# Kernel optimization log

Measured on AMD Instinct MI355X. Metric: run time of the kernel, lower is better.

## Reference

```python
import jax, jax.numpy as jnp
import numpy as np

K = 20
EPS = 1e-5

def knn_idx(x, k):
    # x: (B, N, C). Returns indices of k nearest neighbors (by squared L2), (B, N, k).
    inner = jnp.einsum('bnc,bmc->bnm', x, x)
    sq = jnp.sum(x * x, axis=-1)  # (B, N)
    neg_dist = 2.0 * inner - sq[:, :, None] - sq[:, None, :]
    return jax.lax.top_k(neg_dist, k)[1]

def bn(x, gamma, beta, axes):
    # BatchNorm in training mode (batch statistics, biased variance), eps=1e-5.
    m = jnp.mean(x, axis=axes, keepdims=True)
    v = jnp.var(x, axis=axes, keepdims=True)
    return (x - m) * jax.lax.rsqrt(v + EPS) * gamma + beta

def lrelu(x):
    return jnp.where(x >= 0, x, 0.2 * x)

def edge_conv(x, W, g, b):
    # x: (B, N, C); W: (O, 2C). EdgeConv: knn gather -> concat(nbr-ctr, ctr) -> 1x1 conv -> BN -> LReLU -> max over k.
    B = x.shape[0]
    idx = knn_idx(x, K)                                   # (B, N, K)
    nbr = x[jnp.arange(B)[:, None, None], idx]            # (B, N, K, C)
    ctr = jnp.broadcast_to(x[:, :, None, :], nbr.shape)
    e = jnp.concatenate([nbr - ctr, ctr], axis=-1)        # (B, N, K, 2C)
    h = jnp.einsum('bnkc,oc->bnko', e, W)
    h = lrelu(bn(h, g, b, (0, 1, 2)))
    return jnp.max(h, axis=2)                             # (B, N, O)

def _forward(data, W1, g1, b1, W2, g2, b2, W3, g3, b3, W4, g4, b4,
             W5, g5, b5, fc1W, bn1g, bn1b, fc2W, fc2b, bn2g, bn2b, fc3W, fc3b):
    x = jnp.transpose(data, (0, 2, 1))                    # (B, N, 3)
    d1 = edge_conv(x,  W1, g1, b1)                        # (B, N, 64)
    d2 = edge_conv(d1, W2, g2, b2)                        # (B, N, 64)
    d3 = edge_conv(d2, W3, g3, b3)                        # (B, N, 128)
    d4 = edge_conv(d3, W4, g4, b4)                        # (B, N, 256)
    cat = jnp.concatenate([d1, d2, d3, d4], axis=-1)      # (B, N, 512)
    h = lrelu(bn(jnp.einsum('bnc,oc->bno', cat, W5), g5, b5, (0, 1)))  # (B, N, 1024)
    f = jnp.concatenate([jnp.max(h, axis=1), jnp.mean(h, axis=1)], axis=-1)  # (B, 2048)
    f = lrelu(bn(f @ fc1W.T, bn1g, bn1b, (0,)))           # dropout = identity (eval)
    f = lrelu(bn(f @ fc2W.T + fc2b, bn2g, bn2b, (0,)))
    return f @ fc3W.T + fc3b                              # (B, numClass)

def setup_inputs() -> dict:
    key = jax.random.key(0)
    ks = jax.random.split(key, 16)
    B, N, emb, ncls = 16, 2048, 1024, 40
    s = 0.05
    inp = {
        'data': jax.random.normal(ks[0], (B, 3, N), dtype=jnp.float32),
        'W1': jax.random.normal(ks[1], (64, 6), dtype=jnp.float32) * s,
        'g1': jnp.ones((64,), jnp.float32), 'b1': jnp.zeros((64,), jnp.float32),
        'W2': jax.random.normal(ks[2], (64, 128), dtype=jnp.float32) * s,
        'g2': jnp.ones((64,), jnp.float32), 'b2': jnp.zeros((64,), jnp.float32),
        'W3': jax.random.normal(ks[3], (128, 128), dtype=jnp.float32) * s,
        'g3': jnp.ones((128,), jnp.float32), 'b3': jnp.zeros((128,), jnp.float32),
        'W4': jax.random.normal(ks[4], (256, 256), dtype=jnp.float32) * s,
        'g4': jnp.ones((256,), jnp.float32), 'b4': jnp.zeros((256,), jnp.float32),
        'W5': jax.random.normal(ks[5], (emb, 512), dtype=jnp.float32) * s,
        'g5': jnp.ones((emb,), jnp.float32), 'b5': jnp.zeros((emb,), jnp.float32),
        'fc1W': jax.random.normal(ks[6], (512, emb * 2), dtype=jnp.float32) * s,
        'bn1g': jnp.ones((512,), jnp.float32), 'bn1b': jnp.zeros((512,), jnp.float32),
        'fc2W': jax.random.normal(ks[7], (256, 512), dtype=jnp.float32) * s,
        'fc2b': jnp.zeros((256,), jnp.float32),
        'bn2g': jnp.ones((256,), jnp.float32), 'bn2b': jnp.zeros((256,), jnp.float32),
        'fc3W': jax.random.normal(ks[8], (ncls, 256), dtype=jnp.float32) * s,
        'fc3b': jnp.zeros((ncls,), jnp.float32),
    }
    return inp

def reference(data, W1, g1, b1, W2, g2, b2, W3, g3, b3, W4, g4, b4,
              W5, g5, b5, fc1W, bn1g, bn1b, fc2W, fc2b, bn2g, bn2b, fc3W, fc3b):
    return _forward(data, W1, g1, b1, W2, g2, b2, W3, g3, b3, W4, g4, b4,
                    W5, g5, b5, fc1W, bn1g, bn1b, fc2W, fc2b, bn2g, bn2b, fc3W, fc3b)
```

## Files before the change

### kernel.cpp

```cpp
#include <hip/hip_runtime.h>
#include <math.h>

#define LRELU(x) ((x) >= 0.f ? (x) : 0.2f*(x))

typedef _Float16 f16;
typedef f16 f16x8 __attribute__((ext_vector_type(8)));
typedef f16 f16x4 __attribute__((ext_vector_type(4)));
typedef float f32x4 __attribute__((ext_vector_type(4)));

#define WS_FLOATS 78000000u
__device__ __align__(256) float g_ws[WS_FLOATS];

__global__ __launch_bounds__(256) void k_transpose_in(const float* __restrict__ data,
                                                      float* __restrict__ x0) {
    int i = blockIdx.x*256 + threadIdx.x;
    int b = i >> 11, n = i & 2047;
    #pragma unroll
    for (int c = 0; c < 3; c++)
        x0[(long)i*3 + c] = data[((long)b*3 + c)*2048 + n];
}

__global__ __launch_bounds__(256) void k_sqnorm(const float* __restrict__ x,
                                                float* __restrict__ sq, int C) {
    int i = blockIdx.x*256 + threadIdx.x;
    const float* xr = x + (long)i*C;
    float s = 0.f;
    for (int c = 0; c < C; c++) s = fmaf(xr[c], xr[c], s);
    sq[i] = s;
}

#define KC 8
__global__ __launch_bounds__(256) void k_gemm_nt(
    const float* __restrict__ A, int lda, long sAb,
    const float* __restrict__ B, int ldb, long sBb,
    float* __restrict__ Cm, int ldc, long sCb,
    int K, int Nj, int mode, const float* __restrict__ sq, int sqStride)
{
    __shared__ float As[KC][132];
    __shared__ float Bs[KC][132];
    int z = blockIdx.z;
    const float* Ab = A + (long)z*sAb;
    const float* Bb = B + (long)z*sBb;
    float* Cb = Cm + (long)z*sCb;
    int rowBase = blockIdx.x*128, colBase = blockIdx.y*128;
    int tid = threadIdx.x, tx = tid & 15, ty = tid >> 4;
    float acc[8][8] = {};
    for (int k0 = 0; k0 < K; k0 += KC) {
        #pragma unroll
        for (int l = 0; l < 4; l++) {
            int id = tid + l*256;
            int kk = id & 7, r = id >> 3;
            float av = 0.f, bv = 0.f;
            if (k0 + kk < K) {
                av = Ab[(long)(rowBase + r)*lda + k0 + kk];
                if (colBase + r < Nj)
                    bv = Bb[(long)(colBase + r)*ldb + k0 + kk];
            }
            As[kk][r] = av; Bs[kk][r] = bv;
        }
        __syncthreads();
        #pragma unroll
        for (int kk = 0; kk < KC; kk++) {
            float4 a0 = *(const float4*)&As[kk][ty*8];
            float4 a1 = *(const float4*)&As[kk][ty*8 + 4];
            float4 b0 = *(const float4*)&Bs[kk][tx*4];
            float4 b1 = *(const float4*)&Bs[kk][64 + tx*4];
            float a[8] = {a0.x,a0.y,a0.z,a0.w,a1.x,a1.y,a1.z,a1.w};
            float b[8] = {b0.x,b0.y,b0.z,b0.w,b1.x,b1.y,b1.z,b1.w};
            #pragma unroll
            for (int i = 0; i < 8; i++)
                #pragma unroll
                for (int j = 0; j < 8; j++)
                    acc[i][j] = fmaf(a[i], b[j], acc[i][j]);
        }
        __syncthreads();
    }
    const float* sqz = sq + (long)z*sqStride;
    #pragma unroll
    for (int i = 0; i < 8; i++) {
        int r = rowBase + ty*8 + i;
        float sqr = (mode == 2) ? sqz[r] : 0.f;
        #pragma unroll
        for (int half = 0; half < 2; half++) {
            int c = colBase + half*64 + tx*4;
            int jb = half*4;
            if (c + 3 < Nj) {
                float4 v;
                v.x = acc[i][jb+0]; v.y = acc[i][jb+1];
                v.z = acc[i][jb+2]; v.w = acc[i][jb+3];
                if (mode == 2) {
                    v.x = 2.f*v.x - sqr - sqz[c+0];
                    v.y = 2.f*v.y - sqr - sqz[c+1];
                    v.z = 2.f*v.z - sqr - sqz[c+2];
                    v.w = 2.f*v.w - sqr - sqz[c+3];
                }
                *(float4*)&Cb[(long)r*ldc + c] = v;
            } else {
                #pragma unroll
                for (int j = 0; j < 4; j++) {
                    int c2 = c + j;
                    if (c2 >= Nj) continue;
                    float v = acc[i][jb+j];
                    if (mode == 2) v = 2.f*v - sqr - sqz[c2];
                    Cb[(long)r*ldc + c2] = v;
                }
            }
        }
    }
}

__global__ __launch_bounds__(256) void k_gemm_mfma_nt(
    const f16* __restrict__ A, int lda,
    const f16* __restrict__ Bm, int ldb,
    float* __restrict__ Cm, int ldc, int K)
{
    __shared__ f16 As[128][40];
    __shared__ f16 Bs[128][40];
    int t = threadIdx.x;
    int rowBase = blockIdx.x*128, colBase = blockIdx.y*128;
    int wave = t >> 6, l = t & 63;
    int wrow = (wave >> 1)*64, wcol = (wave & 1)*64;
    int lr = l & 15, kg = l >> 4;
    int sr = t >> 1, seg = (t & 1)*16;

    f32x4 acc[4][4] = {};
    for (int k0 = 0; k0 < K; k0 += 32) {
        const f16* ga = A  + (long)(rowBase + sr)*lda + k0 + seg;
        const f16* gb = Bm + (long)(colBase + sr)*ldb + k0 + seg;
        uint4 a0 = *(const uint4*)ga;
        uint4 a1 = *(const uint4*)(ga + 8);
        uint4 b0 = *(const uint4*)gb;
        uint4 b1 = *(const uint4*)(gb + 8);
        *(uint4*)&As[sr][seg]     = a0;
        *(uint4*)&As[sr][seg + 8] = a1;
        *(uint4*)&Bs[sr][seg]     = b0;
        *(uint4*)&Bs[sr][seg + 8] = b1;
        __syncthreads();
        f16x8 af[4], bf[4];
        #pragma unroll
        for (int i = 0; i < 4; i++) af[i] = *(const f16x8*)&As[wrow + i*16 + lr][kg*8];
        #pragma unroll
        for (int j = 0; j < 4; j++) bf[j] = *(const f16x8*)&Bs[wcol + j*16 + lr][kg*8];
        #pragma unroll
        for (int i = 0; i < 4; i++)
            #pragma unroll
            for (int j = 0; j < 4; j++)
                acc[i][j] = __builtin_amdgcn_mfma_f32_16x16x32_f16(af[i], bf[j], acc[i][j], 0, 0, 0);
        __syncthreads();
    }
    #pragma unroll
    for (int i = 0; i < 4; i++) {
        #pragma unroll
        for (int j = 0; j < 4; j++) {
            int row = rowBase + wrow + i*16 + kg*4;
            int col = colBase + wcol + j*16 + lr;
            #pragma unroll
            for (int r2 = 0; r2 < 4; r2++)
                Cm[(long)(row + r2)*ldc + col] = acc[i][j][r2];
        }
    }
}

__global__ __launch_bounds__(256) void k_cvt_f16(const float* __restrict__ in,
                                                 f16* __restrict__ out, int n) {
    int i = blockIdx.x*256 + threadIdx.x;
    if (i < n) out[i] = (f16)in[i];
}

__global__ __launch_bounds__(256) void k_topk20(const float* __restrict__ dist,
                                                int* __restrict__ idxOut, int rowOffset)
{
    __shared__ float lds[4][2048];
    int wave = threadIdx.x >> 6, lane = threadIdx.x & 63;
    int row = blockIdx.x*4 + wave;
    const float* dr = dist + (long)row*2048;
    float* L = lds[wave];
    for (int i = 0; i < 32; i++) L[i*64 + lane] = dr[i*64 + lane];
    __syncthreads();
    int* out = idxOut + (long)(rowOffset + row)*20;
    for (int it = 0; it < 20; it++) {
        float bv = -INFINITY; int bi = 0x7fffffff;
        for (int i = 0; i < 32; i++) {
            float v = L[i*64 + lane];
            if (v > bv) { bv = v; bi = i*64 + lane; }
        }
        #pragma unroll
        for (int s = 32; s > 0; s >>= 1) {
            float ov = __shfl_xor(bv, s);
            int   oi = __shfl_xor(bi, s);
            if (ov > bv || (ov == bv && oi < bi)) { bv = ov; bi = oi; }
        }
        if (lane == 0) out[it] = bi;
        if (lane == (bi & 63)) L[bi] = -INFINITY;
    }
}

__global__ __launch_bounds__(256) void k_wdiff(const float* __restrict__ W,
                                               float* __restrict__ Wd, int O, int C) {
    int i = blockIdx.x*256 + threadIdx.x;
    if (i >= O*C) return;
    int o = i / C, c = i % C;
    Wd[o*C + c] = W[(long)o*2*C + C + c] - W[(long)o*2*C + c];
}

__global__ __launch_bounds__(256) void k_edge_gather(
    const float* __restrict__ p, const float* __restrict__ q,
    const int* __restrict__ idx,
    float* __restrict__ hmax, float* __restrict__ hmin,
    float* __restrict__ partial, int O, int lg2TPP)
{
    __shared__ float ldsS[1024];
    __shared__ float ldsS2[1024];
    int tid = threadIdx.x;
    int TPP = O >> 2;
    int c4 = (tid & (TPP - 1)) << 2;
    int sub = tid >> lg2TPP;
    int nsub = 256 >> lg2TPP;
    int wg = blockIdx.x;
    int logical = (wg & 7)*256 + (wg >> 3);
    int base = logical*16;
    float4 s = {0,0,0,0}, s2 = {0,0,0,0};
    int iters = 16 / nsub;
    for (int it = 0; it < iters; ++it) {
        int pt = base + sub + it*nsub;
        int bb = (pt >> 11) << 11;
        const int* ir = idx + (long)pt*20;
        float4 qv = *(const float4*)&q[(long)pt*O + c4];
        float4 mx = {-INFINITY,-INFINITY,-INFINITY,-INFINITY};
        float4 mn = { INFINITY, INFINITY, INFINITY, INFINITY};
        for (int k = 0; k < 20; ++k) {
            int m = ir[k];
            float4 pv = *(const float4*)&p[(long)(bb + m)*O + c4];
            float4 h;
            h.x = pv.x + qv.x; h.y = pv.y + qv.y;
            h.z = pv.z + qv.z; h.w = pv.w + qv.w;
            mx.x = fmaxf(mx.x, h.x); mx.y = fmaxf(mx.y, h.y);
            mx.z = fmaxf(mx.z, h.z); mx.w = fmaxf(mx.w, h.w);
            mn.x = fminf(mn.x, h.x); mn.y = fminf(mn.y, h.y);
            mn.z = fminf(mn.z, h.z); mn.w = fminf(mn.w, h.w);
            s.x += h.x; s.y += h.y; s.z += h.z; s.w += h.w;
            s2.x = fmaf(h.x, h.x, s2.x); s2.y = fmaf(h.y, h.y, s2.y);
            s2.z = fmaf(h.z, h.z, s2.z); s2.w = fmaf(h.w, h.w, s2.w);
        }
        *(float4*)&hmax[(long)pt*O + c4] = mx;
        *(float4*)&hmin[(long)pt*O + c4] = mn;
    }
    *(float4*)&ldsS [sub*O + c4] = s;
    *(float4*)&ldsS2[sub*O + c4] = s2;
    __syncthreads();
    if (tid < O) {
        float a = 0.f, b = 0.f;
        for (int u = 0; u < nsub; ++u) { a += ldsS[u*O + tid]; b += ldsS2[u*O + tid]; }
        partial[(long)wg*2*O + tid] = a;
        partial[(long)wg*2*O + O + tid] = b;
    }
}

__global__ __launch_bounds__(256) void k_colsum(const float* __restrict__ partial,
                                                float* __restrict__ out, int W, int rpc) {
    int c = blockIdx.x*256 + threadIdx.x;
    if (c >= W) return;
    long r0 = (long)blockIdx.y * rpc;
    float s = 0.f;
    for (int r = 0; r < rpc; ++r) s += partial[(r0 + r)*W + c];
    out[(long)blockIdx.y*W + c] = s;
}

__global__ __launch_bounds__(256) void k_bn_finalize(
    const float* __restrict__ sums, const float* __restrict__ g,
    const float* __restrict__ beta, float* __restrict__ ss, int O, float invCnt)
{
    int o = blockIdx.x*256 + threadIdx.x;
    if (o >= O) return;
    float mean = sums[o]*invCnt;
    float var  = sums[O + o]*invCnt - mean*mean;
    float sc = g[o] * rsqrtf(var + 1e-5f);
    ss[o] = sc;
    ss[O + o] = beta[o] - mean*sc;
}

__global__ __launch_bounds__(256) void k_edge_apply(
    const float* __restrict__ hmax, const float* __restrict__ hmin,
    const float* __restrict__ ss, float* __restrict__ out, int O,
    f16* __restrict__ catH, int co, int lg2O)
{
    long i4 = (long)blockIdx.x*256 + threadIdx.x;
    int c4 = (int)(i4 & ((O >> 2) - 1)) << 2;
    int pt = (int)(i4 >> (lg2O - 2));
    float4 mx = *(const float4*)&hmax[i4*4];
    float4 mn = *(const float4*)&hmin[i4*4];
    float4 y;
    {
        float sc = ss[c4+0], sh = ss[O+c4+0];
        float v = fmaf(sc >= 0.f ? mx.x : mn.x, sc, sh); y.x = LRELU(v);
    }
    {
        float sc = ss[c4+1], sh = ss[O+c4+1];
        float v = fmaf(sc >= 0.f ? mx.y : mn.y, sc, sh); y.y = LRELU(v);
    }
    {
        float sc = ss[c4+2], sh = ss[O+c4+2];
        float v = fmaf(sc >= 0.f ? mx.z : mn.z, sc, sh); y.z = LRELU(v);
    }
    {
        float sc = ss[c4+3], sh = ss[O+c4+3];
        float v = fmaf(sc >= 0.f ? mx.w : mn.w, sc, sh); y.w = LRELU(v);
    }
    *(float4*)&out[i4*4] = y;
    f16x4 hv;
    hv[0] = (f16)y.x; hv[1] = (f16)y.y; hv[2] = (f16)y.z; hv[3] = (f16)y.w;
    *(f16x4*)&catH[(long)pt*512 + co + c4] = hv;
}

__global__ __launch_bounds__(256) void k_h5_stats_p(const float* __restrict__ h5,
                                                    float* __restrict__ partial) {
    int tid = threadIdx.x, bid = blockIdx.x;
    int base = bid*16;
    float s[4] = {0,0,0,0}, s2[4] = {0,0,0,0};
    for (int i = 0; i < 16; ++i) {
        long row = (long)(base + i)*1024;
        #pragma unroll
        for (int cc = 0; cc < 4; ++cc) {
            float v = h5[row + cc*256 + tid];
            s[cc] += v; s2[cc] = fmaf(v, v, s2[cc]);
        }
    }
    #pragma unroll
    for (int cc = 0; cc < 4; ++cc) {
        partial[(long)bid*2048 + cc*256 + tid] = s[cc];
        partial[(long)bid*2048 + 1024 + cc*256 + tid] = s2[cc];
    }
}

__global__ __launch_bounds__(256) void k_reduce_fp(const float* __restrict__ h5,
                                                   const float* __restrict__ ss,
                                                   float* __restrict__ fpart) {
    int b = blockIdx.x, ch = blockIdx.y;
    int c = blockIdx.z*256 + threadIdx.x;
    float sc = ss[c], sh = ss[1024 + c];
    float mx = -INFINITY, sm = 0.f;
    int n0 = ch*128;
    for (int n = n0; n < n0 + 128; ++n) {
        float v = h5[((long)(b*2048 + n))*1024 + c];
        float y = fmaf(v, sc, sh); y = LRELU(y);
        mx = fmaxf(mx, y); sm += y;
    }
    fpart[((long)(b*16 + ch))*2048 + c] = mx;
    fpart[((long)(b*16 + ch))*2048 + 1024 + c] = sm;
}

__global__ __launch_bounds__(256) void k_reduce_ff(const float* __restrict__ fpart,
                                                   float* __restrict__ f) {
    int b = blockIdx.x;
    int c = blockIdx.y*256 + threadIdx.x;
    float mx = -INFINITY, sm = 0.f;
    for (int ch = 0; ch < 16; ++ch) {
        mx = fmaxf(mx, fpart[((long)(b*16 + ch))*2048 + c]);
        sm += fpart[((long)(b*16 + ch))*2048 + 1024 + c];
    }
    f[(long)b*2048 + c] = mx;
    f[(long)b*2048 + 1024 + c] = sm * (1.f/2048.f);
}

__global__ __launch_bounds__(256) void k_fc_wave(const float* __restrict__ X,
                                                 const float* __restrict__ W,
                                                 const float* __restrict__ bias,
                                                 float* __restrict__ Y,
                                                 int Kdim, int Ncol) {
    int wid = blockIdx.x*4 + (threadIdx.x >> 6);
    int lane = threadIdx.x & 63;
    if (wid >= 16*Ncol) return;
    int b = wid / Ncol, j = wid % Ncol;
    const float* xr = X + (long)b*Kdim;
    const float* wr = W + (long)j*Kdim;
    float s = 0.f;
    for (int k = lane*4; k < Kdim; k += 256) {
        float4 xv = *(const float4*)&xr[k];
        float4 wv = *(const float4*)&wr[k];
        s = fmaf(xv.x, wv.x, s); s = fmaf(xv.y, wv.y, s);
        s = fmaf(xv.z, wv.z, s); s = fmaf(xv.w, wv.w, s);
    }
    #pragma unroll
    for (int sft = 32; sft > 0; sft >>= 1) s += __shfl_xor(s, sft);
    if (lane == 0) Y[wid] = s + (bias ? bias[j] : 0.f);
}

__global__ __launch_bounds__(256) void k_bn_rows(const float* __restrict__ X,
                                                 const float* __restrict__ g,
                                                 const float* __restrict__ be,
                                                 float* __restrict__ Y, int Ncol) {
    int j = blockIdx.x*256 + threadIdx.x;
    if (j >= Ncol) return;
    float s = 0.f, s2 = 0.f;
    for (int b = 0; b < 16; b++) { float v = X[b*Ncol + j]; s += v; s2 = fmaf(v, v, s2); }
    float mean = s*(1.f/16.f);
    float var  = s2*(1.f/16.f) - mean*mean;
    float sc = g[j]*rsqrtf(var + 1e-5f);
    float sh = be[j] - mean*sc;
    for (int b = 0; b < 16; b++) {
        float v = fmaf(X[b*Ncol + j], sc, sh);
        Y[b*Ncol + j] = LRELU(v);
    }
}

extern "C" void kernel_launch(void* const* d_in, const int* in_sizes, int n_in,
                              void* d_out, int out_size, void* d_ws, size_t ws_size,
                              hipStream_t stream) {
    const float* data = (const float*)d_in[0];
    const float* W1 = (const float*)d_in[1];  const float* g1 = (const float*)d_in[2];  const float* b1 = (const float*)d_in[3];
    const float* W2 = (const float*)d_in[4];  const float* g2 = (const float*)d_in[5];  const float* b2 = (const float*)d_in[6];
    const float* W3 = (const float*)d_in[7];  const float* g3 = (const float*)d_in[8];  const float* b3 = (const float*)d_in[9];
    const float* W4 = (const float*)d_in[10]; const float* g4 = (const float*)d_in[11]; const float* b4 = (const float*)d_in[12];
    const float* W5 = (const float*)d_in[13]; const float* g5 = (const float*)d_in[14]; const float* b5 = (const float*)d_in[15];
    const float* fc1W = (const float*)d_in[16]; const float* bn1g = (const float*)d_in[17]; const float* bn1b = (const float*)d_in[18];
    const float* fc2W = (const float*)d_in[19]; const float* fc2b = (const float*)d_in[20];
    const float* bn2g = (const float*)d_in[21]; const float* bn2b = (const float*)d_in[22];
    const float* fc3W = (const float*)d_in[23]; const float* fc3b = (const float*)d_in[24];

    void* wsym = nullptr;
    hipGetSymbolAddress(&wsym, HIP_SYMBOL(g_ws));
    char* w = (char*)wsym;
    size_t off = 0;
    auto alloc = [&](size_t bytes) { void* r = w + off; off += (bytes + 255) & ~size_t(255); return r; };
    float* S   = (float*)alloc(134217728);
    float* x0  = (float*)alloc(393216);
    float* d1  = (float*)alloc(8388608);
    float* d2  = (float*)alloc(8388608);
    float* d3  = (float*)alloc(16777216);
    float* d4  = (float*)alloc(33554432);
    float* p   = (float*)alloc(33554432);
    float* q   = (float*)alloc(33554432);
    int*   idxb= (int*)  alloc(2621440);
    float* sqb = (float*)alloc(131072);
    float* Wd  = (float*)alloc(131072);
    float* sums= (float*)alloc(8192);
    float* ssb = (float*)alloc(8192);
    float* f   = (float*)alloc(131072);
    float* t1  = (float*)alloc(32768);
    float* a1  = (float*)alloc(32768);
    float* t2  = (float*)alloc(16384);
    float* a2  = (float*)alloc(16384);
    f16*  catH = (f16*) alloc(33554432);
    f16*  W5H  = (f16*) alloc(1048576);
    (void)ws_size; (void)n_in; (void)in_sizes; (void)out_size; (void)d_ws;

    float* hmaxb = S;
    float* hminb = S + 8388608;
    float* partb = S + 16777216;
    float* part2 = S + 18874368;
    float* h5par = d4;
    float* h5pt2 = d2;
    float* fpart = d1;

    k_transpose_in<<<128, 256, 0, stream>>>(data, x0);

    auto layer = [&](const float* x, int C, int O, int lg2TPP, int lg2O, int co,
                     const float* W, const float* g, const float* beta, float* out) {
        k_sqnorm<<<128, 256, 0, stream>>>(x, sqb, C);
        for (int ch = 0; ch < 4; ch++) {
            const float* xc = x + (long)ch*8192*C;
            k_gemm_nt<<<dim3(16,16,4), 256, 0, stream>>>(
                xc, C, (long)2048*C, xc, C, (long)2048*C,
                S, 2048, (long)2048*2048, C, 2048, 2, sqb + ch*8192, 2048);
            k_topk20<<<2048, 256, 0, stream>>>(S, idxb, ch*8192);
        }
        k_wdiff<<<(O*C + 255)/256, 256, 0, stream>>>(W, Wd, O, C);
        k_gemm_nt<<<dim3(256, (O+127)/128, 1), 256, 0, stream>>>(
            x, C, 0, W, 2*C, 0, p, O, 0, C, O, 0, nullptr, 0);
        k_gemm_nt<<<dim3(256, (O+127)/128, 1), 256, 0, stream>>>(
            x, C, 0, Wd, C, 0, q, O, 0, C, O, 0, nullptr, 0);
        k_edge_gather<<<2048, 256, 0, stream>>>(p, q, idxb, hmaxb, hminb, partb, O, lg2TPP);
        k_colsum<<<dim3((2*O + 255)/256, 32), 256, 0, stream>>>(partb, part2, 2*O, 64);
        k_colsum<<<dim3((2*O + 255)/256, 1),  256, 0, stream>>>(part2, sums,  2*O, 32);
        k_bn_finalize<<<(O+255)/256, 256, 0, stream>>>(sums, g, beta, ssb, O, 1.f/655360.f);
        k_edge_apply<<<32*O, 256, 0, stream>>>(hmaxb, hminb, ssb, out, O, catH, co, lg2O);
    };

    layer(x0, 3,   64,  4, 6, 0,   W1, g1, b1, d1);
    layer(d1, 64,  64,  4, 6, 64,  W2, g2, b2, d2);
    layer(d2, 64,  128, 5, 7, 128, W3, g3, b3, d3);
    layer(d3, 128, 256, 6, 8, 256, W4, g4, b4, d4);

    k_cvt_f16<<<2048, 256, 0, stream>>>(W5, W5H, 524288);
    k_gemm_mfma_nt<<<dim3(256, 8), 256, 0, stream>>>(catH, 512, W5H, 512, S, 1024, 512);

    k_h5_stats_p<<<2048, 256, 0, stream>>>(S, h5par);
    k_colsum<<<dim3(8, 32), 256, 0, stream>>>(h5par, h5pt2, 2048, 64);
    k_colsum<<<dim3(8, 1),  256, 0, stream>>>(h5pt2, sums,  2048, 32);
    k_bn_finalize<<<4, 256, 0, stream>>>(sums, g5, b5, ssb, 1024, 1.f/32768.f);
    k_reduce_fp<<<dim3(16,16,4), 256, 0, stream>>>(S, ssb, fpart);
    k_reduce_ff<<<dim3(16,4), 256, 0, stream>>>(fpart, f);

    k_fc_wave<<<2048, 256, 0, stream>>>(f,  fc1W, nullptr, t1, 2048, 512);
    k_bn_rows<<<2, 256, 0, stream>>>(t1, bn1g, bn1b, a1, 512);
    k_fc_wave<<<1024, 256, 0, stream>>>(a1, fc2W, fc2b, t2, 512, 256);
    k_bn_rows<<<1, 256, 0, stream>>>(t2, bn2g, bn2b, a2, 256);
    k_fc_wave<<<160, 256, 0, stream>>>(a2, fc3W, fc3b, (float*)d_out, 256, 40);
}
```

Baseline: 2.194 ms.

## Fuse kNN distance GEMM with top-k selection in shared memory

Replaces the per-chunk distance GEMM plus separate top-20 kernel with one fused kernel. It computes an 8-row tile of pairwise distances against a transposed copy of x, keeps the tile in LDS and runs the top-k selection there. This removes writing and re-reading the full 2048x2048 distance matrix in global memory, and cuts four chunk launches down to one. The fused GEMM is a plain FMA loop with lower reuse than the tiled GEMM, and it uses 64KB of LDS per block, which limits occupancy. It also adds a transpose kernel and a larger workspace.

Result: slower. 3.864 ms (+76.1%).

```diff
diff --git a/kernel.cpp b/kernel.cpp
--- a/kernel.cpp
+++ b/kernel.cpp
@@ -8,7 +8,7 @@
 typedef f16 f16x4 __attribute__((ext_vector_type(4)));
 typedef float f32x4 __attribute__((ext_vector_type(4)));
 
-#define WS_FLOATS 78000000u
+#define WS_FLOATS 92000000u
 __device__ __align__(256) float g_ws[WS_FLOATS];
 
 __global__ __launch_bounds__(256) void k_transpose_in(const float* __restrict__ data,
@@ -27,6 +27,118 @@
     float s = 0.f;
     for (int c = 0; c < C; c++) s = fmaf(xr[c], xr[c], s);
     sq[i] = s;
+}
+
+__global__ __launch_bounds__(256) void k_transpose_xT(const float* __restrict__ x,
+                                                      float* __restrict__ xT,
+                                                      int C, int KP) {
+    long id = (long)blockIdx.x*256 + threadIdx.x;
+    int n = (int)(id & 2047);
+    long t = id >> 11;
+    int k = (int)(t % KP);
+    int b = (int)(t / KP);
+    xT[((long)b*128 + k)*2048 + n] = (k < C) ? x[((long)(b << 11) + n)*C + k] : 0.f;
+}
+
+__global__ __launch_bounds__(256) void k_knn_fused(
+    const float* __restrict__ x,
+    const float* __restrict__ xT,
+    const float* __restrict__ sq,
+    int* __restrict__ idxOut,
+    int C, int KP)
+{
+    __shared__ float distL[8][2048];
+    int tid = threadIdx.x;
+    int b = blockIdx.y;
+    const float* xTb = xT + (long)b*128*2048;
+    const float* sqb2 = sq + (b << 11);
+    int tx = tid & 15;
+    int ry = tid >> 4;
+    int rp = ry & 3;
+    int g  = ry >> 2;
+    int wave = tid >> 6, lane = tid & 63;
+
+    for (int rb = 0; rb < 8; ++rb) {
+        int rbase = blockIdx.x*64 + rb*8;
+        int r0 = rbase + 2*rp, r1 = r0 + 1;
+        const float* xr0 = x + ((long)(b << 11) + r0)*C;
+        const float* xr1 = x + ((long)(b << 11) + r1)*C;
+        float sqr0 = sqb2[r0], sqr1 = sqb2[r1];
+        for (int ct = 0; ct < 8; ++ct) {
+            int c0 = ct*256 + g*64 + tx*4;
+            float4 acc0 = {0,0,0,0}, acc1 = {0,0,0,0};
+            for (int k0 = 0; k0 < KP; k0 += 8) {
+                float4 bv[8];
+                #pragma unroll
+                for (int kk = 0; kk < 8; ++kk)
+                    bv[kk] = *(const float4*)&xTb[(long)(k0 + kk)*2048 + c0];
+                float a0v[8], a1v[8];
+                if (C >= 8) {
+                    float4 t0 = *(const float4*)&xr0[k0];
+                    float4 t1 = *(const float4*)&xr0[k0 + 4];
+                    a0v[0]=t0.x; a0v[1]=t0.y; a0v[2]=t0.z; a0v[3]=t0.w;
+                    a0v[4]=t1.x; a0v[5]=t1.y; a0v[6]=t1.z; a0v[7]=t1.w;
+                    float4 u0 = *(const float4*)&xr1[k0];
+                    float4 u1 = *(const float4*)&xr1[k0 + 4];
+                    a1v[0]=u0.x; a1v[1]=u0.y; a1v[2]=u0.z; a1v[3]=u0.w;
+                    a1v[4]=u1.x; a1v[5]=u1.y; a1v[6]=u1.z; a1v[7]=u1.w;
+                } else {
+                    #pragma unroll
+                    for (int kk = 0; kk < 8; ++kk) {
+                        int k = k0 + kk;
+                        a0v[kk] = (k < C) ? xr0[k] : 0.f;
+                        a1v[kk] = (k < C) ? xr1[k] : 0.f;
+                    }
+                }
+                #pragma unroll
+                for (int kk = 0; kk < 8; ++kk) {
+                    float4 bb = bv[kk];
+                    acc0.x = fmaf(a0v[kk], bb.x, acc0.x);
+                    acc0.y = fmaf(a0v[kk], bb.y, acc0.y);
+                    acc0.z = fmaf(a0v[kk], bb.z, acc0.z);
+                    acc0.w = fmaf(a0v[kk], bb.w, acc0.w);
+                    acc1.x = fmaf(a1v[kk], bb.x, acc1.x);
+                    acc1.y = fmaf(a1v[kk], bb.y, acc1.y);
+                    acc1.z = fmaf(a1v[kk], bb.z, acc1.z);
+                    acc1.w = fmaf(a1v[kk], bb.w, acc1.w);
+                }
+            }
+            float4 sqc = *(const float4*)&sqb2[c0];
+            float4 d0, d1v;
+            d0.x  = 2.f*acc0.x - sqr0 - sqc.x;
+            d0.y  = 2.f*acc0.y - sqr0 - sqc.y;
+            d0.z  = 2.f*acc0.z - sqr0 - sqc.z;
+            d0.w  = 2.f*acc0.w - sqr0 - sqc.w;
+            d1v.x = 2.f*acc1.x - sqr1 - sqc.x;
+            d1v.y = 2.f*acc1.y - sqr1 - sqc.y;
+            d1v.z = 2.f*acc1.z - sqr1 - sqc.z;
+            d1v.w = 2.f*acc1.w - sqr1 - sqc.w;
+            *(float4*)&distL[2*rp][c0]     = d0;
+            *(float4*)&distL[2*rp + 1][c0] = d1v;
+        }
+        __syncthreads();
+        for (int t = 0; t < 2; ++t) {
+            int r = wave*2 + t;
+            float* L = distL[r];
+            int* out = idxOut + ((long)(b << 11) + rbase + r)*20;
+            for (int it = 0; it < 20; ++it) {
+                float bvv = -INFINITY; int bi = 0x7fffffff;
+                for (int i = 0; i < 32; ++i) {
+                    float v = L[i*64 + lane];
+                    if (v > bvv) { bvv = v; bi = i*64 + lane; }
+                }
+                #pragma unroll
+                for (int s = 32; s > 0; s >>= 1) {
+                    float ov = __shfl_xor(bvv, s);
+                    int   oi = __shfl_xor(bi, s);
+                    if (ov > bvv || (ov == bvv && oi < bi)) { bvv = ov; bi = oi; }
+                }
+                if (lane == 0) out[it] = bi;
+                if (lane == (bi & 63)) L[bi] = -INFINITY;
+            }
+        }
+        __syncthreads();
+    }
 }
 
 #define KC 8
@@ -165,34 +277,6 @@
                                                  f16* __restrict__ out, int n) {
     int i = blockIdx.x*256 + threadIdx.x;
     if (i < n) out[i] = (f16)in[i];
-}
-
-__global__ __launch_bounds__(256) void k_topk20(const float* __restrict__ dist,
-                                                int* __restrict__ idxOut, int rowOffset)
-{
-    __shared__ float lds[4][2048];
-    int wave = threadIdx.x >> 6, lane = threadIdx.x & 63;
-    int row = blockIdx.x*4 + wave;
-    const float* dr = dist + (long)row*2048;
-    float* L = lds[wave];
-    for (int i = 0; i < 32; i++) L[i*64 + lane] = dr[i*64 + lane];
-    __syncthreads();
-    int* out = idxOut + (long)(rowOffset + row)*20;
-    for (int it = 0; it < 20; it++) {
-        float bv = -INFINITY; int bi = 0x7fffffff;
-        for (int i = 0; i < 32; i++) {
-            float v = L[i*64 + lane];
-            if (v > bv) { bv = v; bi = i*64 + lane; }
-        }
-        #pragma unroll
-        for (int s = 32; s > 0; s >>= 1) {
-            float ov = __shfl_xor(bv, s);
-            int   oi = __shfl_xor(bi, s);
-            if (ov > bv || (ov == bv && oi < bi)) { bv = ov; bi = oi; }
-        }
-        if (lane == 0) out[it] = bi;
-        if (lane == (bi & 63)) L[bi] = -INFINITY;
-    }
 }
 
 __global__ __launch_bounds__(256) void k_wdiff(const float* __restrict__ W,
@@ -442,12 +526,14 @@
     float* a2  = (float*)alloc(16384);
     f16*  catH = (f16*) alloc(33554432);
     f16*  W5H  = (f16*) alloc(1048576);
+    float* xT  = (float*)alloc(16777216);
     (void)ws_size; (void)n_in; (void)in_sizes; (void)out_size; (void)d_ws;
 
     float* hmaxb = S;
     float* hminb = S + 8388608;
     float* partb = S + 16777216;
     float* part2 = S + 18874368;
+    float* h5    = S;
     float* h5par = d4;
     float* h5pt2 = d2;
     float* fpart = d1;
@@ -456,14 +542,10 @@
 
     auto layer = [&](const float* x, int C, int O, int lg2TPP, int lg2O, int co,
                      const float* W, const float* g, const float* beta, float* out) {
+        int KP = ((C + 7) >> 3) << 3;
         k_sqnorm<<<128, 256, 0, stream>>>(x, sqb, C);
-        for (int ch = 0; ch < 4; ch++) {
-            const float* xc = x + (long)ch*8192*C;
-            k_gemm_nt<<<dim3(16,16,4), 256, 0, stream>>>(
-                xc, C, (long)2048*C, xc, C, (long)2048*C,
-                S, 2048, (long)2048*2048, C, 2048, 2, sqb + ch*8192, 2048);
-            k_topk20<<<2048, 256, 0, stream>>>(S, idxb, ch*8192);
-        }
+        k_transpose_xT<<<KP*128, 256, 0, stream>>>(x, xT, C, KP);
+        k_knn_fused<<<dim3(32, 16), 256, 0, stream>>>(x, xT, sqb, idxb, C, KP);
         k_wdiff<<<(O*C + 255)/256, 256, 0, stream>>>(W, Wd, O, C);
         k_gemm_nt<<<dim3(256, (O+127)/128, 1), 256, 0, stream>>>(
             x, C, 0, W, 2*C, 0, p, O, 0, C, O, 0, nullptr, 0);
@@ -482,13 +564,13 @@
     layer(d3, 128, 256, 6, 8, 256, W4, g4, b4, d4);
 
     k_cvt_f16<<<2048, 256, 0, stream>>>(W5, W5H, 524288);
-    k_gemm_mfma_nt<<<dim3(256, 8), 256, 0, stream>>>(catH, 512, W5H, 512, S, 1024, 512);
-
-    k_h5_stats_p<<<2048, 256, 0, stream>>>(S, h5par);
+    k_gemm_mfma_nt<<<dim3(256, 8), 256, 0, stream>>>(catH, 512, W5H, 512, h5, 1024, 512);
+
+    k_h5_stats_p<<<2048, 256, 0, stream>>>(h5, h5par);
     k_colsum<<<dim3(8, 32), 256, 0, stream>>>(h5par, h5pt2, 2048, 64);
     k_colsum<<<dim3(8, 1),  256, 0, stream>>>(h5pt2, sums,  2048, 32);
     k_bn_finalize<<<4, 256, 0, stream>>>(sums, g5, b5, ssb, 1024, 1.f/32768.f);
-    k_reduce_fp<<<dim3(16,16,4), 256, 0, stream>>>(S, ssb, fpart);
+    k_reduce_fp<<<dim3(16,16,4), 256, 0, stream>>>(h5, ssb, fpart);
     k_reduce_ff<<<dim3(16,4), 256, 0, stream>>>(fpart, f);
 
     k_fc_wave<<<2048, 256, 0, stream>>>(f,  fc1W, nullptr, t1, 2048, 512);
```

## Fuse distance GEMM with per-tile top-k and add candidate merge kernel

Applied to the files above, without the earlier changes.

Replaces the chunked distance GEMM plus per-row top-k over a full 2048x2048 distance matrix with one fused kernel. Each 128x128 tile computes distances and selects a 20-candidate list per row for its column block using cross-lane shuffles. A second kernel merges the 16 candidate lists (320 entries) per row into the final 20 neighbors. This avoids writing and reading the full distance matrix and the LDS-based scan over 2048 entries, at the cost of 20 serial shuffle-reduction rounds per row inside the GEMM epilogue.

New measurement: 6.251 ms. +184.9%, slower.

```diff
diff --git a/kernel.cpp b/kernel.cpp
--- a/kernel.cpp
+++ b/kernel.cpp
@@ -30,6 +30,119 @@
 }
 
 #define KC 8
+__global__ __launch_bounds__(256) void k_gemm_topk(
+    const float* __restrict__ X, int C, const float* __restrict__ sq,
+    float* __restrict__ candV, int* __restrict__ candI)
+{
+    __shared__ float As[KC][132];
+    __shared__ float Bs[KC][132];
+    int z = blockIdx.z;
+    const float* Ab = X + ((long)z << 11)*C;
+    int rowBase = blockIdx.x*128, colBase = blockIdx.y*128;
+    int tid = threadIdx.x, tx = tid & 15, ty = tid >> 4;
+    float acc[8][8] = {};
+    for (int k0 = 0; k0 < C; k0 += KC) {
+        #pragma unroll
+        for (int l = 0; l < 4; l++) {
+            int id = tid + l*256;
+            int kk = id & 7, r = id >> 3;
+            float av = 0.f, bv = 0.f;
+            if (k0 + kk < C) {
+                av = Ab[(long)(rowBase + r)*C + k0 + kk];
+                bv = Ab[(long)(colBase + r)*C + k0 + kk];
+            }
+            As[kk][r] = av; Bs[kk][r] = bv;
+        }
+        __syncthreads();
+        #pragma unroll
+        for (int kk = 0; kk < KC; kk++) {
+            float4 a0 = *(const float4*)&As[kk][ty*8];
+            float4 a1 = *(const float4*)&As[kk][ty*8 + 4];
+            float4 b0 = *(const float4*)&Bs[kk][tx*4];
+            float4 b1 = *(const float4*)&Bs[kk][64 + tx*4];
+            float a[8] = {a0.x,a0.y,a0.z,a0.w,a1.x,a1.y,a1.z,a1.w};
+            float b[8] = {b0.x,b0.y,b0.z,b0.w,b1.x,b1.y,b1.z,b1.w};
+            #pragma unroll
+            for (int i = 0; i < 8; i++)
+                #pragma unroll
+                for (int j = 0; j < 8; j++)
+                    acc[i][j] = fmaf(a[i], b[j], acc[i][j]);
+        }
+        __syncthreads();
+    }
+    const float* sqz = sq + ((long)z << 11);
+    #pragma unroll
+    for (int i = 0; i < 8; i++) {
+        int rloc = ty*8 + i;
+        float sqr = sqz[rowBase + rloc];
+        float dv[8]; int gi[8];
+        #pragma unroll
+        for (int j = 0; j < 8; j++) {
+            int c = colBase + ((j < 4) ? tx*4 + j : 64 + tx*4 + (j - 4));
+            dv[j] = 2.f*acc[i][j] - sqr - sqz[c];
+            gi[j] = c;
+        }
+        unsigned mask = 0;
+        long obase = (((long)((z << 11) + rowBase + rloc))*16 + blockIdx.y)*20;
+        for (int it = 0; it < 20; it++) {
+            float bv = -INFINITY; int bi = 0x7fffffff;
+            #pragma unroll
+            for (int j = 0; j < 8; j++) {
+                if (!((mask >> j) & 1u)) {
+                    if (dv[j] > bv || (dv[j] == bv && gi[j] < bi)) { bv = dv[j]; bi = gi[j]; }
+                }
+            }
+            #pragma unroll
+            for (int sft = 1; sft < 16; sft <<= 1) {
+                float ov = __shfl_xor(bv, sft);
+                int   oi = __shfl_xor(bi, sft);
+                if (ov > bv || (ov == bv && oi < bi)) { bv = ov; bi = oi; }
+            }
+            #pragma unroll
+            for (int j = 0; j < 8; j++)
+                if (gi[j] == bi) mask |= 1u << j;
+            if (tx == 0) { candV[obase + it] = bv; candI[obase + it] = bi; }
+        }
+    }
+}
+
+__global__ __launch_bounds__(256) void k_topk_merge(
+    const float* __restrict__ candV, const int* __restrict__ candI,
+    int* __restrict__ idxOut)
+{
+    int wave = threadIdx.x >> 6, lane = threadIdx.x & 63;
+    int row = blockIdx.x*4 + wave;
+    const float* cv = candV + (long)row*320;
+    const int*   ci = candI + (long)row*320;
+    float v[5]; int id[5];
+    #pragma unroll
+    for (int u = 0; u < 5; u++) {
+        v[u]  = cv[lane + u*64];
+        id[u] = ci[lane + u*64];
+    }
+    unsigned mask = 0;
+    int* out = idxOut + (long)row*20;
+    for (int it = 0; it < 20; it++) {
+        float bv = -INFINITY; int bi = 0x7fffffff;
+        #pragma unroll
+        for (int u = 0; u < 5; u++) {
+            if (!((mask >> u) & 1u)) {
+                if (v[u] > bv || (v[u] == bv && id[u] < bi)) { bv = v[u]; bi = id[u]; }
+            }
+        }
+        #pragma unroll
+        for (int sft = 32; sft > 0; sft >>= 1) {
+            float ov = __shfl_xor(bv, sft);
+            int   oi = __shfl_xor(bi, sft);
+            if (ov > bv || (ov == bv && oi < bi)) { bv = ov; bi = oi; }
+        }
+        #pragma unroll
+        for (int u = 0; u < 5; u++)
+            if (id[u] == bi) mask |= 1u << u;
+        if (lane == 0) out[it] = bi;
+    }
+}
+
 __global__ __launch_bounds__(256) void k_gemm_nt(
     const float* __restrict__ A, int lda, long sAb,
     const float* __restrict__ B, int ldb, long sBb,
@@ -165,34 +278,6 @@
                                                  f16* __restrict__ out, int n) {
     int i = blockIdx.x*256 + threadIdx.x;
     if (i < n) out[i] = (f16)in[i];
-}
-
-__global__ __launch_bounds__(256) void k_topk20(const float* __restrict__ dist,
-                                                int* __restrict__ idxOut, int rowOffset)
-{
-    __shared__ float lds[4][2048];
-    int wave = threadIdx.x >> 6, lane = threadIdx.x & 63;
-    int row = blockIdx.x*4 + wave;
-    const float* dr = dist + (long)row*2048;
-    float* L = lds[wave];
-    for (int i = 0; i < 32; i++) L[i*64 + lane] = dr[i*64 + lane];
-    __syncthreads();
-    int* out = idxOut + (long)(rowOffset + row)*20;
-    for (int it = 0; it < 20; it++) {
-        float bv = -INFINITY; int bi = 0x7fffffff;
-        for (int i = 0; i < 32; i++) {
-            float v = L[i*64 + lane];
-            if (v > bv) { bv = v; bi = i*64 + lane; }
-        }
-        #pragma unroll
-        for (int s = 32; s > 0; s >>= 1) {
-            float ov = __shfl_xor(bv, s);
-            int   oi = __shfl_xor(bi, s);
-            if (ov > bv || (ov == bv && oi < bi)) { bv = ov; bi = oi; }
-        }
-        if (lane == 0) out[it] = bi;
-        if (lane == (bi & 63)) L[bi] = -INFINITY;
-    }
 }
 
 __global__ __launch_bounds__(256) void k_wdiff(const float* __restrict__ W,
@@ -418,7 +503,7 @@
     const float* fc3W = (const float*)d_in[23]; const float* fc3b = (const float*)d_in[24];
 
     void* wsym = nullptr;
-    hipGetSymbolAddress(&wsym, HIP_SYMBOL(g_ws));
+    (void)hipGetSymbolAddress(&wsym, HIP_SYMBOL(g_ws));
     char* w = (char*)wsym;
     size_t off = 0;
     auto alloc = [&](size_t bytes) { void* r = w + off; off += (bytes + 255) & ~size_t(255); return r; };
@@ -444,6 +529,8 @@
     f16*  W5H  = (f16*) alloc(1048576);
     (void)ws_size; (void)n_in; (void)in_sizes; (void)out_size; (void)d_ws;
 
+    float* candV = S;
+    int*   candI = (int*)(S + 10485760);
     float* hmaxb = S;
     float* hminb = S + 8388608;
     float* partb = S + 16777216;
@@ -457,13 +544,8 @@
     auto layer = [&](const float* x, int C, int O, int lg2TPP, int lg2O, int co,
                      const float* W, const float* g, const float* beta, float* out) {
         k_sqnorm<<<128, 256, 0, stream>>>(x, sqb, C);
-        for (int ch = 0; ch < 4; ch++) {
-            const float* xc = x + (long)ch*8192*C;
-            k_gemm_nt<<<dim3(16,16,4), 256, 0, stream>>>(
-                xc, C, (long)2048*C, xc, C, (long)2048*C,
-                S, 2048, (long)2048*2048, C, 2048, 2, sqb + ch*8192, 2048);
-            k_topk20<<<2048, 256, 0, stream>>>(S, idxb, ch*8192);
-        }
+        k_gemm_topk<<<dim3(16,16,16), 256, 0, stream>>>(x, C, sqb, candV, candI);
+        k_topk_merge<<<8192, 256, 0, stream>>>(candV, candI, idxb);
         k_wdiff<<<(O*C + 255)/256, 256, 0, stream>>>(W, Wd, O, C);
         k_gemm_nt<<<dim3(256, (O+127)/128, 1), 256, 0, stream>>>(
             x, C, 0, W, 2*C, 0, p, O, 0, C, O, 0, nullptr, 0);
```
